# Kernel optimization log

Hardware: AMD Instinct MI355X
Metric: run time of the kernel (lower is better)

## Reference

```python
import jax, jax.numpy as jnp
import numpy as np

B, S, D = 2, 2048, 2048
H, HKV, HD = 32, 8, 64          # query heads, kv heads, head dim (GQA factor 4)
WIN = 1024                       # sliding_window_length
QKV_DIM = HD * (H + 2 * HKV)     # 3072


def setup_inputs() -> dict:
    key = jax.random.key(0)
    k0, k1, k2, k3, k4 = jax.random.split(key, 5)
    x = jax.random.normal(k0, (B, S, D), dtype=jnp.float32)
    Wqkv = jax.random.normal(k1, (QKV_DIM, D), dtype=jnp.float32) * 0.02
    bqkv = jax.random.normal(k2, (QKV_DIM,), dtype=jnp.float32) * 0.02
    Wout = jax.random.normal(k3, (D, H * HD), dtype=jnp.float32) * 0.02
    bout = jax.random.normal(k4, (D,), dtype=jnp.float32) * 0.02
    return {"x": x, "Wqkv": Wqkv, "bqkv": bqkv, "Wout": Wout, "bout": bout}


def reference(x, Wqkv, bqkv, Wout, bout):
    rep = H // HKV
    scale = 1.0 / np.sqrt(HD).astype(np.float32)
    # in_proj (torch Linear: y = x @ W.T + b)
    qkv = jnp.einsum('bsd,ed->bse', x, Wqkv) + bqkv          # [B,S,QKV_DIM]
    q = qkv[..., : H * HD].reshape(B, S, HKV, rep, HD)        # grouped query heads
    kv = qkv[..., H * HD:].reshape(B, S, 2, HKV, HD)
    k, v = kv[:, :, 0], kv[:, :, 1]                           # [B,S,HKV,HD]
    # GQA attention without materializing repeated K/V: group query heads per kv head
    scores = jnp.einsum('bqgrd,bkgd->bgrqk', q, k) * scale    # [B,HKV,rep,S,S]
    i = jnp.arange(S)[:, None]
    j = jnp.arange(S)[None, :]
    mask = (j <= i) & (j > i - WIN)
    scores = jnp.where(mask, scores, -jnp.inf)
    attn = jax.nn.softmax(scores, axis=-1)
    ctx = jnp.einsum('bgrqk,bkgd->bqgrd', attn, v)            # [B,S,HKV,rep,HD]
    ctx = ctx.reshape(B, S, H * HD)
    out = jnp.einsum('bse,de->bsd', ctx, Wout) + bout
    return out
```

## Files before the change

### kernel.cpp

```cpp
#include <hip/hip_runtime.h>
#include <stdint.h>

#define S_LEN   2048
#define D_MODEL 2048
#define NH      32
#define NKV     8
#define HDIM    64
#define WIN     1024
#define QKV_N   3072
#define MTOT    4096
#define QSCALE  0.18033688011112042f

typedef __bf16 bf16x8 __attribute__((ext_vector_type(8)));
typedef float  f32x4  __attribute__((ext_vector_type(4)));
typedef unsigned short u16x8 __attribute__((ext_vector_type(8)));
typedef unsigned short u16x4 __attribute__((ext_vector_type(4)));

#define GLDS16(g, l) __builtin_amdgcn_global_load_lds( \
    (__attribute__((address_space(1))) void*)(g),      \
    (__attribute__((address_space(3))) void*)(l), 16, 0, 0)

__device__ __forceinline__ unsigned short f2bf(float f) {
  __bf16 b = (__bf16)f;
  return __builtin_bit_cast(unsigned short, b);
}

__global__ void cvt3(const float* __restrict__ s0, unsigned short* __restrict__ d0, int n0,
                     const float* __restrict__ s1, unsigned short* __restrict__ d1, int n1,
                     const float* __restrict__ s2, unsigned short* __restrict__ d2, int n2)
{
  int total4 = (n0 + n1 + n2) >> 2;
  for (int idx = blockIdx.x * blockDim.x + threadIdx.x; idx < total4;
       idx += gridDim.x * blockDim.x) {
    int i = idx << 2;
    const float* s; unsigned short* d;
    if (i < n0)            { s = s0 + i;            d = d0 + i; }
    else if (i < n0 + n1)  { s = s1 + (i - n0);     d = d1 + (i - n0); }
    else                   { s = s2 + (i - n0 - n1); d = d2 + (i - n0 - n1); }
    float4 v = *(const float4*)s;
    u16x4 o;
    o[0] = f2bf(v.x); o[1] = f2bf(v.y); o[2] = f2bf(v.z); o[3] = f2bf(v.w);
    *(u16x4*)d = o;
  }
}

template<int EP>
__global__ __launch_bounds__(256)
void gemm_nt(const unsigned short* __restrict__ A, const unsigned short* __restrict__ Bm,
             const float* __restrict__ bias, int K, int N,
             unsigned short* __restrict__ qo, unsigned short* __restrict__ ko,
             unsigned short* __restrict__ vo, float* __restrict__ co)
{
  __shared__ __align__(16) char smem[(EP == 0) ? 36864 : 16384];
  unsigned short* sA = (unsigned short*)smem;
  unsigned short* sB = (unsigned short*)(smem + 8192);

  const int t = threadIdx.x;
  const int l = t & 63;
  const int brow = blockIdx.y << 7;
  const int bcol = blockIdx.x << 7;
  const int wr = ((t >> 7) & 1) << 6;
  const int wc = ((t >> 6) & 1) << 6;

  const int srow  = t >> 2;
  const int skoff = (t & 3) << 3;
  const unsigned short* aP = A + (size_t)(brow + srow) * K + skoff;
  const unsigned short* bP = Bm + (size_t)(bcol + srow) * K + skoff;
  unsigned short* ldsA0 = sA + ((t & 192) << 3);
  unsigned short* ldsA1 = sA + ((256 + (t & 192)) << 3);
  unsigned short* ldsB0 = sB + ((t & 192) << 3);
  unsigned short* ldsB1 = sB + ((256 + (t & 192)) << 3);

  f32x4 acc[4][4] = {};
  const int fr = l & 15;
  const int fk = (l >> 4) << 3;

  for (int kt = 0; kt < K; kt += 32) {
    GLDS16(aP, ldsA0);
    GLDS16(aP + (size_t)64 * K, ldsA1);
    GLDS16(bP, ldsB0);
    GLDS16(bP + (size_t)64 * K, ldsB1);
    aP += 32; bP += 32;
    __syncthreads();

    bf16x8 af[4], bf[4];
#pragma unroll
    for (int mi = 0; mi < 4; ++mi)
      af[mi] = *(const bf16x8*)&sA[(wr + mi * 16 + fr) * 32 + fk];
#pragma unroll
    for (int ni = 0; ni < 4; ++ni)
      bf[ni] = *(const bf16x8*)&sB[(wc + ni * 16 + fr) * 32 + fk];
#pragma unroll
    for (int mi = 0; mi < 4; ++mi)
#pragma unroll
      for (int ni = 0; ni < 4; ++ni)
        acc[mi][ni] = __builtin_amdgcn_mfma_f32_16x16x32_bf16(af[mi], bf[ni], acc[mi][ni], 0, 0, 0);
    __syncthreads();
  }

  const int fq4 = (l >> 4) << 2;
  if (EP == 0) {
    const int w2 = t >> 6;
    const int e0 = bcol + wc;
    const int m0 = brow + wr;
    const int bidx = m0 >> 11, s0 = m0 & 2047;
    unsigned short* tile = (unsigned short*)smem + w2 * (64 * 72);
    const float sc = (e0 < 2048) ? QSCALE : 1.0f;
    const bool isV = (e0 >= 2560);
#pragma unroll
    for (int ni = 0; ni < 4; ++ni) {
      const int dd = ni * 16 + fr;
      const float bs = bias[e0 + dd];
#pragma unroll
      for (int mi = 0; mi < 4; ++mi)
#pragma unroll
        for (int j = 0; j < 4; ++j) {
          const int mm = mi * 16 + fq4 + j;
          const float v = (acc[mi][ni][j] + bs) * sc;
          if (isV) tile[dd * 72 + mm] = f2bf(v);
          else     tile[mm * 72 + dd] = f2bf(v);
        }
    }
    const int lr = l >> 3, lc = l & 7;
    unsigned short* gbase;
    size_t rstride;
    if (e0 < 2048) {
      gbase = qo + (((size_t)bidx * NH + (e0 >> 6)) * S_LEN + s0) * HDIM;
      rstride = HDIM;
    } else if (e0 < 2560) {
      gbase = ko + (((size_t)bidx * NKV + ((e0 - 2048) >> 6)) * S_LEN + s0) * HDIM;
      rstride = HDIM;
    } else {
      gbase = vo + (((size_t)bidx * NKV + ((e0 - 2560) >> 6)) * HDIM) * (size_t)S_LEN + s0;
      rstride = S_LEN;
    }
#pragma unroll
    for (int p = 0; p < 8; ++p) {
      const int row = p * 8 + lr;
      u16x8 vv = *(const u16x8*)&tile[row * 72 + lc * 8];
      *(u16x8*)(gbase + (size_t)row * rstride + lc * 8) = vv;
    }
  } else {
#pragma unroll
    for (int mi = 0; mi < 4; ++mi)
#pragma unroll
      for (int j = 0; j < 4; ++j) {
        const int m = brow + wr + mi * 16 + fq4 + j;
#pragma unroll
        for (int ni = 0; ni < 4; ++ni) {
          const int n = bcol + wc + ni * 16 + fr;
          co[(size_t)m * N + n] = acc[mi][ni][j] + bias[n];
        }
      }
  }
}

__global__ __launch_bounds__(512)
void attn_swin(const unsigned short* __restrict__ Qs, const unsigned short* __restrict__ Kb,
               const unsigned short* __restrict__ Vtb, unsigned short* __restrict__ ctx)
{
  __shared__ char lds[32768];

  const int t = threadIdx.x, w = t >> 6, l = t & 63;
  const int fr = l & 15, fq = l >> 4;
  const int qh = w & 3, kh = w >> 2;
  const int q0 = blockIdx.x << 6;
  const int h = blockIdx.y, b = blockIdx.z;
  const int g = h >> 2;

  const unsigned short* qp = Qs + (((size_t)(b * NH + h)) * S_LEN + q0 + (qh << 4)) * HDIM;
  const bf16x8 qf0 = *(const bf16x8*)(qp + fr * HDIM + (fq << 3));
  const bf16x8 qf1 = *(const bf16x8*)(qp + fr * HDIM + 32 + (fq << 3));

  const unsigned short* Kg  = Kb  + ((size_t)(b * NKV + g)) * S_LEN * HDIM;
  const unsigned short* Vtg = Vtb + ((size_t)(b * NKV + g)) * HDIM * S_LEN;

  float m_run = -1e30f, l_part = 0.0f;
  f32x4 o_acc[4] = {};

  int lo = q0 - (WIN - 1); if (lo < 0) lo = 0; lo &= ~63;
  const int hi = q0 + 64;
  const int full_lo = q0 - (WIN - 64);
  const int full_hi = q0 - 64;

  const unsigned short* src0;
  const unsigned short* src1;
  {
    const int x0 = ((w & 3) << 11) + (l << 4);
    const int x1 = x0 + 1024;
    if (w < 4) {
      const int s0 = x0 >> 7, o0 = ((x0 >> 4) & 7) ^ (s0 & 7);
      const int s1 = x1 >> 7, o1 = ((x1 >> 4) & 7) ^ (s1 & 7);
      const int p0 = ((s0 >> 5) << 5) | (((s0 >> 2) & 3) << 3) | (((s0 >> 4) & 1) << 2) | (s0 & 3);
      const int p1 = ((s1 >> 5) << 5) | (((s1 >> 2) & 3) << 3) | (((s1 >> 4) & 1) << 2) | (s1 & 3);
      src0 = Kg + (size_t)(lo + p0) * HDIM + (o0 << 3);
      src1 = Kg + (size_t)(lo + p1) * HDIM + (o1 << 3);
    } else {
      const int d0 = x0 >> 7, o0 = ((x0 >> 4) & 7) ^ (d0 & 7);
      const int d1 = x1 >> 7, o1 = ((x1 >> 4) & 7) ^ (d1 & 7);
      src0 = Vtg + (size_t)d0 * S_LEN + lo + (o0 << 3);
      src1 = Vtg + (size_t)d1 * S_LEN + lo + (o1 << 3);
    }
  }
  const int sadv = (w < 4) ? 64 * HDIM : 64;
  const int dbase = ((w < 4) ? 0 : 8192) + ((w & 3) << 11) + (l << 4);

  char* bufA = lds;
  char* bufB = lds + 16384;

  GLDS16(src0, bufA + dbase);
  GLDS16(src1, bufA + dbase + 1024);
  src0 += sadv; src1 += sadv;

  const int iq = q0 + (qh << 4) + fr;
  const int swr = (fr & 7) << 4;

  auto TILE = [&](int kv0, const char* sK, const char* sV, bool MASKED)
      __attribute__((always_inline)) {
    bf16x8 kf[2][2];
#pragma unroll
    for (int ntg = 0; ntg < 2; ++ntg) {
      const int slot = (kh << 5) + (ntg << 4) + fr;
      kf[ntg][0] = *(const bf16x8*)(sK + (((slot << 7) + (fq << 4)) ^ swr));
      kf[ntg][1] = *(const bf16x8*)(sK + (((slot << 7) + ((fq + 4) << 4)) ^ swr));
    }
    __builtin_amdgcn_s_setprio(1);
    f32x4 sf[2];
#pragma unroll
    for (int ntg = 0; ntg < 2; ++ntg) {
      f32x4 z = {};
      z = __builtin_amdgcn_mfma_f32_16x16x32_bf16(kf[ntg][0], qf0, z, 0, 0, 0);
      z = __builtin_amdgcn_mfma_f32_16x16x32_bf16(kf[ntg][1], qf1, z, 0, 0, 0);
      sf[ntg] = z;
    }
    __builtin_amdgcn_s_setprio(0);
    if (MASKED) {
#pragma unroll
      for (int ntg = 0; ntg < 2; ++ntg)
#pragma unroll
        for (int r = 0; r < 4; ++r) {
          const int jk = kv0 + (kh << 5) + (fq << 3) + (ntg << 2) + r;
          if (jk > iq || jk <= iq - WIN) sf[ntg][r] = -1e30f;
        }
    }
    float pmax;
    {
      f32x4 mx = sf[0];
      mx[0] = fmaxf(mx[0], sf[1][0]); mx[1] = fmaxf(mx[1], sf[1][1]);
      mx[2] = fmaxf(mx[2], sf[1][2]); mx[3] = fmaxf(mx[3], sf[1][3]);
      pmax = fmaxf(fmaxf(mx[0], mx[1]), fmaxf(mx[2], mx[3]));
    }
    if (__any(pmax - m_run > 8.0f)) {
      float rmax = fmaxf(pmax, __shfl_xor(pmax, 16));
      rmax = fmaxf(rmax, __shfl_xor(rmax, 32));
      const float mnew = fmaxf(m_run, rmax);
      const float rs = exp2f(m_run - mnew);
      m_run = mnew;
      l_part *= rs;
      float rs_o[4];
#pragma unroll
      for (int r = 0; r < 4; ++r) rs_o[r] = __shfl(rs, (fq << 2) + r, 16);
#pragma unroll
      for (int dt = 0; dt < 4; ++dt)
#pragma unroll
        for (int r = 0; r < 4; ++r) o_acc[dt][r] *= rs_o[r];
    }
    union { unsigned short us[8]; bf16x8 v; } pu;
    float lloc = 0.0f;
#pragma unroll
    for (int ntg = 0; ntg < 2; ++ntg)
#pragma unroll
      for (int r = 0; r < 4; ++r) {
        const float p = exp2f(sf[ntg][r] - m_run);
        lloc += p;
        pu.us[(ntg << 2) + r] = f2bf(p);
      }
    l_part += lloc;
    bf16x8 vf[4];
#pragma unroll
    for (int dt = 0; dt < 4; ++dt) {
      const int d = (dt << 4) + fr;
      vf[dt] = *(const bf16x8*)(sV + ((d << 7) + ((((kh << 2) + fq) ^ (fr & 7)) << 4)));
    }
    __builtin_amdgcn_s_setprio(1);
#pragma unroll
    for (int dt = 0; dt < 4; ++dt)
      o_acc[dt] = __builtin_amdgcn_mfma_f32_16x16x32_bf16(pu.v, vf[dt], o_acc[dt], 0, 0, 0);
    __builtin_amdgcn_s_setprio(0);
  };

  for (int kv0 = lo; kv0 < hi; kv0 += 64) {
    __syncthreads();
    if (kv0 + 64 < hi) {
      GLDS16(src0, bufB + dbase);
      GLDS16(src1, bufB + dbase + 1024);
      src0 += sadv; src1 += sadv;
    }
    const bool masked = (kv0 < full_lo) || (kv0 > full_hi);
    if (masked) TILE(kv0, bufA, bufA + 8192, true);
    else        TILE(kv0, bufA, bufA + 8192, false);
    char* tmp = bufA; bufA = bufB; bufB = tmp;
  }

  float lsum = l_part;
  lsum += __shfl_xor(lsum, 16);
  lsum += __shfl_xor(lsum, 32);

  __syncthreads();
  if (w < 4) {
    char* ob = lds + ((w & 3) << 12);
#pragma unroll
    for (int dt = 0; dt < 4; ++dt)
      *(f32x4*)(ob + (dt << 10) + (l << 4)) = o_acc[dt];
    if (fq == 0) {
      *(float*)(lds + 16384 + ((w & 3) << 7) + (fr << 3))     = m_run;
      *(float*)(lds + 16384 + ((w & 3) << 7) + (fr << 3) + 4) = lsum;
    }
  }
  __syncthreads();
  if (w >= 4) {
    const char* ob = lds + ((w & 3) << 12);
    const float m_p = *(const float*)(lds + 16384 + ((w & 3) << 7) + (fr << 3));
    const float l_p = *(const float*)(lds + 16384 + ((w & 3) << 7) + (fr << 3) + 4);
    const float m_f = fmaxf(m_run, m_p);
    const float a  = exp2f(m_run - m_f);
    const float bb = exp2f(m_p  - m_f);
    const float inv = 1.0f / (a * lsum + bb * l_p);
    const float alpha = a * inv, beta = bb * inv;
    float al[4], be[4];
#pragma unroll
    for (int r = 0; r < 4; ++r) {
      al[r] = __shfl(alpha, (fq << 2) + r, 16);
      be[r] = __shfl(beta,  (fq << 2) + r, 16);
    }
    unsigned short* cp = ctx + ((size_t)(b * S_LEN + q0 + (qh << 4))) * D_MODEL + h * HDIM;
#pragma unroll
    for (int dt = 0; dt < 4; ++dt) {
      const f32x4 op = *(const f32x4*)(ob + (dt << 10) + (l << 4));
#pragma unroll
      for (int r = 0; r < 4; ++r) {
        const float of = al[r] * o_acc[dt][r] + be[r] * op[r];
        cp[(size_t)((fq << 2) + r) * D_MODEL + (dt << 4) + fr] = f2bf(of);
      }
    }
  }
}

extern "C" void kernel_launch(void* const* d_in, const int* in_sizes, int n_in,
                              void* d_out, int out_size, void* d_ws, size_t ws_size,
                              hipStream_t stream)
{
  const float* x    = (const float*)d_in[0];
  const float* Wqkv = (const float*)d_in[1];
  const float* bqkv = (const float*)d_in[2];
  const float* Wout = (const float*)d_in[3];
  const float* bout = (const float*)d_in[4];
  float* out = (float*)d_out;

  char* ws = (char*)d_ws;
  if (ws_size < 62914560u) return;

  unsigned short* xb    = (unsigned short*)(ws);
  unsigned short* ctx   = xb;
  unsigned short* wqkvb = (unsigned short*)(ws + 16777216);
  unsigned short* woutb = (unsigned short*)(ws + 29360128);
  unsigned short* Qs    = (unsigned short*)(ws + 37748736);
  unsigned short* Kbuf  = (unsigned short*)(ws + 54525952);
  unsigned short* Vtbuf = (unsigned short*)(ws + 58720256);

  cvt3<<<2048, 256, 0, stream>>>(x, xb, MTOT * D_MODEL,
                                 Wqkv, wqkvb, QKV_N * D_MODEL,
                                 Wout, woutb, D_MODEL * D_MODEL);

  gemm_nt<0><<<dim3(QKV_N / 128, MTOT / 128), 256, 0, stream>>>(
      xb, wqkvb, bqkv, D_MODEL, QKV_N, Qs, Kbuf, Vtbuf, nullptr);

  attn_swin<<<dim3(S_LEN / 64, NH, 2), 512, 0, stream>>>(Qs, Kbuf, Vtbuf, ctx);

  gemm_nt<1><<<dim3(D_MODEL / 128, MTOT / 128), 256, 0, stream>>>(
      ctx, woutb, bout, D_MODEL, D_MODEL, nullptr, nullptr, nullptr, out);
}
```

Before: 219.9 us.

## Triple-buffer K/V tiles in attention with explicit vmcnt waits

Grows the attention kernel's LDS staging from two to three 16KB buffers so that K/V tiles are prefetched two iterations ahead via global_load_lds. The loop waits only for the oldest in-flight tile with a partial s_waitcnt vmcnt(2) before a barrier, rather than relying on a full __syncthreads drain. This aims to hide more global-load latency behind the MFMA work. In exchange it uses 48KB of LDS per block, which may reduce occupancy, and it depends on the hand-written vmcnt counts being correct.

```diff
diff --git a/kernel.cpp b/kernel.cpp
--- a/kernel.cpp
+++ b/kernel.cpp
@@ -23,6 +23,13 @@
 __device__ __forceinline__ unsigned short f2bf(float f) {
   __bf16 b = (__bf16)f;
   return __builtin_bit_cast(unsigned short, b);
+}
+
+__device__ __forceinline__ void hard_barrier() {
+  asm volatile("" ::: "memory");
+  __builtin_amdgcn_s_barrier();
+  asm volatile("" ::: "memory");
+  __builtin_amdgcn_sched_barrier(0);
 }
 
 __global__ void cvt3(const float* __restrict__ s0, unsigned short* __restrict__ d0, int n0,
@@ -159,7 +166,7 @@
 void attn_swin(const unsigned short* __restrict__ Qs, const unsigned short* __restrict__ Kb,
                const unsigned short* __restrict__ Vtb, unsigned short* __restrict__ ctx)
 {
-  __shared__ char lds[32768];
+  __shared__ char lds[49152];
 
   const int t = threadIdx.x, w = t >> 6, l = t & 63;
   const int fr = l & 15, fq = l >> 4;
@@ -205,12 +212,9 @@
   const int sadv = (w < 4) ? 64 * HDIM : 64;
   const int dbase = ((w < 4) ? 0 : 8192) + ((w & 3) << 11) + (l << 4);
 
-  char* bufA = lds;
-  char* bufB = lds + 16384;
-
-  GLDS16(src0, bufA + dbase);
-  GLDS16(src1, bufA + dbase + 1024);
-  src0 += sadv; src1 += sadv;
+  char* bA = lds;
+  char* bB = lds + 16384;
+  char* bC = lds + 32768;
 
   const int iq = q0 + (qh << 4) + fr;
   const int swr = (fr & 7) << 4;
@@ -289,17 +293,28 @@
     __builtin_amdgcn_s_setprio(0);
   };
 
+  GLDS16(src0, bA + dbase);
+  GLDS16(src1, bA + dbase + 1024);
+  src0 += sadv; src1 += sadv;
+  if (lo + 64 < hi) {
+    GLDS16(src0, bB + dbase);
+    GLDS16(src1, bB + dbase + 1024);
+    src0 += sadv; src1 += sadv;
+  }
+
   for (int kv0 = lo; kv0 < hi; kv0 += 64) {
-    __syncthreads();
-    if (kv0 + 64 < hi) {
-      GLDS16(src0, bufB + dbase);
-      GLDS16(src1, bufB + dbase + 1024);
+    if (kv0 + 64 < hi) asm volatile("s_waitcnt vmcnt(2)" ::: "memory");
+    else               asm volatile("s_waitcnt vmcnt(0)" ::: "memory");
+    hard_barrier();
+    if (kv0 + 128 < hi) {
+      GLDS16(src0, bC + dbase);
+      GLDS16(src1, bC + dbase + 1024);
       src0 += sadv; src1 += sadv;
     }
     const bool masked = (kv0 < full_lo) || (kv0 > full_hi);
-    if (masked) TILE(kv0, bufA, bufA + 8192, true);
-    else        TILE(kv0, bufA, bufA + 8192, false);
-    char* tmp = bufA; bufA = bufB; bufB = tmp;
+    if (masked) TILE(kv0, bA, bA + 8192, true);
+    else        TILE(kv0, bA, bA + 8192, false);
+    char* tmp = bA; bA = bB; bB = bC; bC = tmp;
   }
 
   float lsum = l_part;
```

After: 221.2 us. About the same (+0.6%).
